# Kernel tuning notes

Hardware: AMD Instinct MI355X
Metric: run time of the kernel (lower is better)

Reference implementation:

```python
import jax, jax.numpy as jnp
import numpy as np

B, S, D, H, E = 4, 1024, 1024, 4096, 8


def setup_inputs() -> dict:
    key = jax.random.key(0)
    ks = jax.random.split(key, 5)
    sd = 1.0 / np.sqrt(D)
    sh = 1.0 / np.sqrt(H)
    x = jax.random.normal(ks[0], (B, S, D), dtype=jnp.float32)
    # stacked expert weights: Linear(D->H), ReLU, Linear(H->D)
    W1 = jax.random.normal(ks[1], (E, D, H), dtype=jnp.float32) * sd
    b1 = jnp.zeros((E, H), dtype=jnp.float32)
    W2 = jax.random.normal(ks[2], (E, H, D), dtype=jnp.float32) * sh
    b2 = jnp.zeros((E, D), dtype=jnp.float32)
    # gate Linear(D->E)
    Wg = jax.random.normal(ks[3], (D, E), dtype=jnp.float32) * sd
    bg = jnp.zeros((E,), dtype=jnp.float32)
    return {"x": x, "W1": W1, "b1": b1, "W2": W2, "b2": b2,
            "Wg": Wg, "bg": bg, "top_k": 2}


def reference(x, W1, b1, W2, b2, Wg, bg, top_k):
    # gating
    gating_scores = jnp.einsum('bsd,de->bse', x, Wg) + bg          # [B,S,E]
    gating_probs = jax.nn.softmax(gating_scores, axis=-1)
    _, top_k_indices = jax.lax.top_k(gating_probs, top_k)          # [B,S,K]
    n_exp = Wg.shape[1]
    # per-token 0/1 mask of selected experts (matches torch sum over k of mask)
    # NOTE: original code multiplies by the binary mask only; top_k_probs are
    # computed but NOT used as combine weights. We reproduce that faithfully.
    sel = jnp.sum(top_k_indices[..., None] == jnp.arange(n_exp), axis=2)  # [B,S,E]
    sel = sel.astype(x.dtype)
    # dense all-experts FFN (as the original does)
    h = jax.nn.relu(jnp.einsum('bsd,edh->bseh', x, W1) + b1)       # [B,S,E,H]
    eo = jnp.einsum('bseh,ehd->bsed', h, W2) + b2                  # [B,S,E,D]
    output = jnp.einsum('bsed,bse->bsd', eo, sel)                  # [B,S,D]
    return (output, gating_scores)
```

## Files before the change

### kernel.cpp

```cpp
#include <hip/hip_runtime.h>
#include <hip/hip_bf16.h>
#include <stdint.h>

#define B_ 4
#define S_ 1024
#define D_ 1024
#define H_ 4096
#define E_ 8
#define T_ (B_*S_)

#define GBM 128
#define BK 64
#define MAXT1 2432
#define MAXT2 1280

typedef __bf16 bf16x8 __attribute__((ext_vector_type(8)));
typedef float f32x4 __attribute__((ext_vector_type(4)));
typedef unsigned short ushort8 __attribute__((ext_vector_type(8)));
typedef unsigned short ushort4v __attribute__((ext_vector_type(4)));

__device__ __forceinline__ unsigned short f2bf(float f) {
  union { float f; uint32_t u; } v; v.f = f;
  uint32_t u = v.u;
  u += 0x7fff + ((u >> 16) & 1);
  return (unsigned short)(u >> 16);
}

__device__ __forceinline__ void gl16(const void* g, void* l) {
  __builtin_amdgcn_global_load_lds(
      (const __attribute__((address_space(1))) void*)g,
      (__attribute__((address_space(3))) void*)l,
      16, 0, 0);
}

__global__ __launch_bounds__(256) void transpose_conv(
    const float* __restrict__ in, unsigned short* __restrict__ outp,
    int R, int C) {
  __shared__ unsigned short tile[64][66];
  const int e = blockIdx.z;
  const size_t eoff = (size_t)e * R * C;
  const int r0 = blockIdx.y * 64, c0 = blockIdx.x * 64;
  const int t = threadIdx.x;
  {
    const int r = t >> 2, cseg = (t & 3) * 16;
    const float4* s4 = (const float4*)(in + eoff + (size_t)(r0 + r) * C + (c0 + cseg));
    float4 v0 = s4[0], v1 = s4[1], v2 = s4[2], v3 = s4[3];
    ushort8 w0, w1;
    w0[0]=f2bf(v0.x); w0[1]=f2bf(v0.y); w0[2]=f2bf(v0.z); w0[3]=f2bf(v0.w);
    w0[4]=f2bf(v1.x); w0[5]=f2bf(v1.y); w0[6]=f2bf(v1.z); w0[7]=f2bf(v1.w);
    w1[0]=f2bf(v2.x); w1[1]=f2bf(v2.y); w1[2]=f2bf(v2.z); w1[3]=f2bf(v2.w);
    w1[4]=f2bf(v3.x); w1[5]=f2bf(v3.y); w1[6]=f2bf(v3.z); w1[7]=f2bf(v3.w);
    *(ushort8*)&tile[r][cseg]     = w0;
    *(ushort8*)&tile[r][cseg + 8] = w1;
  }
  __syncthreads();
  {
    const int c = t >> 2, rseg = (t & 3) * 16;
    ushort8 w0, w1;
#pragma unroll
    for (int j = 0; j < 8; ++j) {
      w0[j] = tile[rseg + j][c];
      w1[j] = tile[rseg + 8 + j][c];
    }
    unsigned short* dst = outp + eoff + (size_t)(c0 + c) * R + (r0 + rseg);
    *(ushort8*)dst       = w0;
    *(ushort8*)(dst + 8) = w1;
  }
}

__global__ __launch_bounds__(256) void gating_kernel(
    const float* __restrict__ x, const float* __restrict__ Wg,
    const float* __restrict__ bg, float* __restrict__ scores,
    unsigned short* __restrict__ xb,
    int* __restrict__ cnt, int* __restrict__ lists) {
  int t = blockIdx.x * 4 + (threadIdx.x >> 6);
  int l = threadIdx.x & 63;
  float acc[E_];
#pragma unroll
  for (int e = 0; e < E_; ++e) acc[e] = 0.f;
  const float* xr = x + (size_t)t * D_;
  unsigned short* xbr = xb + (size_t)t * D_;
  for (int k4 = l * 4; k4 < D_; k4 += 256) {
    float4 xv = *(const float4*)(xr + k4);
    ushort4v wq;
    wq[0] = f2bf(xv.x); wq[1] = f2bf(xv.y); wq[2] = f2bf(xv.z); wq[3] = f2bf(xv.w);
    *(ushort4v*)(xbr + k4) = wq;
#pragma unroll
    for (int q = 0; q < 4; ++q) {
      float xs = (q == 0) ? xv.x : (q == 1) ? xv.y : (q == 2) ? xv.z : xv.w;
      const float4* w = (const float4*)(Wg + (size_t)(k4 + q) * E_);
      float4 w0 = w[0], w1 = w[1];
      acc[0] += xs * w0.x; acc[1] += xs * w0.y; acc[2] += xs * w0.z; acc[3] += xs * w0.w;
      acc[4] += xs * w1.x; acc[5] += xs * w1.y; acc[6] += xs * w1.z; acc[7] += xs * w1.w;
    }
  }
#pragma unroll
  for (int off = 32; off > 0; off >>= 1)
#pragma unroll
    for (int e = 0; e < E_; ++e) acc[e] += __shfl_xor(acc[e], off, 64);
  if (l == 0) {
    float s[E_];
#pragma unroll
    for (int e = 0; e < E_; ++e) {
      s[e] = acc[e] + bg[e];
      scores[(size_t)t * E_ + e] = s[e];
    }
    int i1 = 0; float m1 = -1e30f;
#pragma unroll
    for (int e = 0; e < E_; ++e) if (s[e] > m1) { m1 = s[e]; i1 = e; }
    int i2 = -1; float m2 = -1e30f;
#pragma unroll
    for (int e = 0; e < E_; ++e) if (e != i1 && s[e] > m2) { m2 = s[e]; i2 = e; }
    int p1 = atomicAdd(&cnt[i1], 1); lists[i1 * T_ + p1] = t;
    int p2 = atomicAdd(&cnt[i2], 1); lists[i2 * T_ + p2] = t;
  }
}

__global__ void scan_kernel(const int* __restrict__ cnt, int* __restrict__ off,
                            int* __restrict__ hdr, int* __restrict__ t1tab,
                            int* __restrict__ t2tab) {
  if (threadIdx.x == 0) {
    int o = 0;
    int mtiles[E_];
    for (int e = 0; e < E_; ++e) {
      off[e] = o; o += cnt[e];
      mtiles[e] = (cnt[e] + GBM - 1) / GBM;
    }
    int n1 = 0;
    for (int e = 0; e < E_; ++e)
      for (int nt = 0; nt < H_ / GBM; ++nt)
        for (int mt = 0; mt < mtiles[e]; ++mt)
          t1tab[n1++] = (e << 16) | (mt << 8) | nt;
    int n2 = 0;
    for (int e = 0; e < E_; ++e)
      for (int sp = 0; sp < 2; ++sp)
        for (int nt = 0; nt < D_ / GBM; ++nt)
          for (int mt = 0; mt < mtiles[e]; ++mt)
            t2tab[n2++] = (e << 16) | (mt << 8) | (sp << 6) | nt;
    hdr[0] = n1; hdr[1] = n2;
  }
}

template <int LAYER, int SPLITK>
__global__ __launch_bounds__(256, 4) void ffn_gemm(
    const unsigned short* __restrict__ xb,
    const unsigned short* __restrict__ hbuf,
    const unsigned short* __restrict__ WT,
    const float* __restrict__ bias,
    const int* __restrict__ cnt, const int* __restrict__ off,
    const int* __restrict__ lists,
    const int* __restrict__ tab, const int* __restrict__ hdr,
    unsigned short* __restrict__ hout,
    float* __restrict__ out)
{
  constexpr int K = (LAYER == 1) ? D_ : H_;
  constexpr int N = (LAYER == 1) ? H_ : D_;
  constexpr int KS = K / SPLITK;
  constexpr int NT = KS / BK;

  const int ntask = hdr[LAYER - 1];
  const int b = blockIdx.x;
  if (b >= ntask) return;
  const int q = ntask >> 3, r = ntask & 7;
  const int x = b & 7, ii = b >> 3;
  const int task = (x < r ? x * (q + 1) : r * (q + 1) + (x - r) * q) + ii;

  const int ent = tab[task];
  const int e  = ent >> 16;
  const int m0 = ((ent >> 8) & 0xff) * GBM;
  const int sp = (ent >> 6) & 3;
  const int n0 = (ent & 63) * GBM;
  const int k0 = sp * KS;
  const int count = cnt[e];
  const int oe = off[e];
  const int* lst = lists + e * T_;

  __shared__ unsigned short sA[GBM * BK];
  __shared__ unsigned short sB[GBM * BK];

  const int tid  = threadIdx.x;
  const int lane = tid & 63;
  const int wv   = tid >> 6;
  const int wm   = (wv >> 1) * 64;
  const int wn   = (wv & 1) * 64;

  const int srow   = lane >> 3;
  const int schunk = (lane & 7) * 16;
  const int sgoff  = schunk ^ (srow << 4);

  const char* arow[4];
  const char* brow[4];
#pragma unroll
  for (int i = 0; i < 4; ++i) {
    int rr = i * 32 + wv * 8 + srow;
    int gr = m0 + rr;
    if (LAYER == 1) {
      int tok = (gr < count) ? lst[gr] : lst[m0];
      arow[i] = (const char*)(xb + (size_t)tok * K + k0);
    } else {
      int r2 = (gr < count) ? gr : m0;
      arow[i] = (const char*)(hbuf + (size_t)(oe + r2) * K + k0);
    }
    brow[i] = (const char*)(WT + (size_t)e * N * K + (size_t)(n0 + rr) * K + k0);
  }

  const int lrow = lane & 15;
  const int kg   = lane >> 4;
  const int fswz = (lrow & 7) << 4;

  f32x4 acc[4][4];
#pragma unroll
  for (int i = 0; i < 4; ++i)
#pragma unroll
    for (int j = 0; j < 4; ++j) acc[i][j] = (f32x4){0.f, 0.f, 0.f, 0.f};

#pragma unroll 1
  for (int t = 0; t < NT; ++t) {
    const int kb = t * 128;
#pragma unroll
    for (int i = 0; i < 4; ++i)
      gl16(arow[i] + kb + sgoff, (char*)sA + (i * 32 + wv * 8) * 128);
#pragma unroll
    for (int i = 0; i < 4; ++i)
      gl16(brow[i] + kb + sgoff, (char*)sB + (i * 32 + wv * 8) * 128);
    __syncthreads();
#pragma unroll
    for (int ks = 0; ks < 2; ++ks) {
      bf16x8 af[4], bfm[4];
      const int kbyte = ks * 64 + kg * 16;
#pragma unroll
      for (int i = 0; i < 4; ++i) {
        af[i]  = *(const bf16x8*)((const char*)sA + (wm + i * 16 + lrow) * 128 + (kbyte ^ fswz));
        bfm[i] = *(const bf16x8*)((const char*)sB + (wn + i * 16 + lrow) * 128 + (kbyte ^ fswz));
      }
#pragma unroll
      for (int i = 0; i < 4; ++i)
#pragma unroll
        for (int j = 0; j < 4; ++j)
          acc[i][j] = __builtin_amdgcn_mfma_f32_16x16x32_bf16(af[i], bfm[j], acc[i][j], 0, 0, 0);
    }
    __syncthreads();
  }

  const int rbase = 4 * kg;
#pragma unroll
  for (int i = 0; i < 4; ++i) {
#pragma unroll
    for (int r2 = 0; r2 < 4; ++r2) {
      int row  = wm + i * 16 + rbase + r2;
      int grow = m0 + row;
      if (grow < count) {
#pragma unroll
        for (int j = 0; j < 4; ++j) {
          int col  = wn + j * 16 + lrow;
          int gcol = n0 + col;
          float bv = (SPLITK == 1 || sp == 0) ? bias[(size_t)e * N + gcol] : 0.f;
          float v = acc[i][j][r2] + bv;
          if (LAYER == 1) {
            v = v > 0.f ? v : 0.f;
            hout[(size_t)(oe + grow) * H_ + gcol] = f2bf(v);
          } else {
            int tok = lst[grow];
            atomicAdd(&out[(size_t)tok * D_ + gcol], v);
          }
        }
      }
    }
  }
}

extern "C" void kernel_launch(void* const* d_in, const int* in_sizes, int n_in,
                              void* d_out, int out_size, void* d_ws, size_t ws_size,
                              hipStream_t stream) {
  (void)in_sizes; (void)n_in; (void)out_size; (void)ws_size;
  const float* x  = (const float*)d_in[0];
  const float* W1 = (const float*)d_in[1];
  const float* b1 = (const float*)d_in[2];
  const float* W2 = (const float*)d_in[3];
  const float* b2 = (const float*)d_in[4];
  const float* Wg = (const float*)d_in[5];
  const float* bg = (const float*)d_in[6];

  float* out    = (float*)d_out;
  float* scores = out + (size_t)T_ * D_;

  char* ws = (char*)d_ws;
  int* cnt   = (int*)ws;
  int* off   = (int*)(ws + 32);
  int* hdr   = (int*)(ws + 64);
  int* t1tab = (int*)(ws + 128);
  int* t2tab = (int*)(ws + 10240);
  int* lists = (int*)(ws + 16384);
  unsigned short* xb   = (unsigned short*)(ws + 16384 + 131072);
  unsigned short* hbuf = (unsigned short*)(ws + 16384 + 131072 + 8388608);
  unsigned short* WT   = (unsigned short*)(ws + 16384 + 131072 + 8388608 + 67108864);

  hipMemsetAsync(out, 0, (size_t)T_ * D_ * sizeof(float), stream);
  hipMemsetAsync(cnt, 0, 64, stream);

  gating_kernel<<<T_ / 4, 256, 0, stream>>>(x, Wg, bg, scores, xb, cnt, lists);
  scan_kernel<<<1, 64, 0, stream>>>(cnt, off, hdr, t1tab, t2tab);

  transpose_conv<<<dim3(H_ / 64, D_ / 64, E_), 256, 0, stream>>>(W1, WT, D_, H_);
  ffn_gemm<1, 1><<<MAXT1, 256, 0, stream>>>(
      xb, hbuf, WT, b1, cnt, off, lists, t1tab, hdr, hbuf, nullptr);

  transpose_conv<<<dim3(D_ / 64, H_ / 64, E_), 256, 0, stream>>>(W2, WT, H_, D_);
  ffn_gemm<2, 2><<<MAXT2, 256, 0, stream>>>(
      xb, hbuf, WT, b2, cnt, off, lists, t2tab, hdr, nullptr, out);
}
```

Baseline: 492.8 us.

## Widen GEMM tile to 128x256 and load A fragments directly into registers

The grouped FFN GEMM tile grows from 128x128 to 128x256. The A operand is no longer staged in LDS; each wave loads its A fragments straight from global memory into registers, while B is staged through LDS with twice as many rows. The scan kernel now builds each expert's task-table segment in parallel across threads, and launch bounds drop to 2 blocks per SM to make room for the doubled accumulators. The aim is fewer tasks and more reuse of each LDS B tile per K step, at the cost of uncoalesced direct A loads, lower occupancy and coarser load balance.

```diff
diff --git a/kernel.cpp b/kernel.cpp
--- a/kernel.cpp
+++ b/kernel.cpp
@@ -10,9 +10,10 @@
 #define T_ (B_*S_)
 
 #define GBM 128
+#define GBN 256
 #define BK 64
-#define MAXT1 2432
-#define MAXT2 1280
+#define MAXT1 1216
+#define MAXT2 640
 
 typedef __bf16 bf16x8 __attribute__((ext_vector_type(8)));
 typedef float f32x4 __attribute__((ext_vector_type(4)));
@@ -119,30 +120,38 @@
 __global__ void scan_kernel(const int* __restrict__ cnt, int* __restrict__ off,
                             int* __restrict__ hdr, int* __restrict__ t1tab,
                             int* __restrict__ t2tab) {
-  if (threadIdx.x == 0) {
-    int o = 0;
-    int mtiles[E_];
+  const int l = threadIdx.x;
+  int offl[E_], mt[E_];
+  int o = 0;
+  for (int e = 0; e < E_; ++e) {
+    offl[e] = o; o += cnt[e];
+    mt[e] = (cnt[e] + GBM - 1) / GBM;
+  }
+  if (l < E_) {
+    int s1 = 0, s2 = 0;
+    for (int e = 0; e < l; ++e) { s1 += mt[e] * (H_ / GBN); s2 += mt[e] * 2 * (D_ / GBN); }
+    int n1 = s1;
+    for (int nt = 0; nt < H_ / GBN; ++nt)
+      for (int m = 0; m < mt[l]; ++m)
+        t1tab[n1++] = (l << 16) | (m << 8) | nt;
+    int n2 = s2;
+    for (int sp = 0; sp < 2; ++sp)
+      for (int nt = 0; nt < D_ / GBN; ++nt)
+        for (int m = 0; m < mt[l]; ++m)
+          t2tab[n2++] = (l << 16) | (m << 8) | (sp << 6) | nt;
+  }
+  if (l == 0) {
+    int s1 = 0, s2 = 0;
     for (int e = 0; e < E_; ++e) {
-      off[e] = o; o += cnt[e];
-      mtiles[e] = (cnt[e] + GBM - 1) / GBM;
-    }
-    int n1 = 0;
-    for (int e = 0; e < E_; ++e)
-      for (int nt = 0; nt < H_ / GBM; ++nt)
-        for (int mt = 0; mt < mtiles[e]; ++mt)
-          t1tab[n1++] = (e << 16) | (mt << 8) | nt;
-    int n2 = 0;
-    for (int e = 0; e < E_; ++e)
-      for (int sp = 0; sp < 2; ++sp)
-        for (int nt = 0; nt < D_ / GBM; ++nt)
-          for (int mt = 0; mt < mtiles[e]; ++mt)
-            t2tab[n2++] = (e << 16) | (mt << 8) | (sp << 6) | nt;
-    hdr[0] = n1; hdr[1] = n2;
+      s1 += mt[e] * (H_ / GBN); s2 += mt[e] * 2 * (D_ / GBN);
+      off[e] = offl[e];
+    }
+    hdr[0] = s1; hdr[1] = s2;
   }
 }
 
 template <int LAYER, int SPLITK>
-__global__ __launch_bounds__(256, 4) void ffn_gemm(
+__global__ __launch_bounds__(256, 2) void ffn_gemm(
     const unsigned short* __restrict__ xb,
     const unsigned short* __restrict__ hbuf,
     const unsigned short* __restrict__ WT,
@@ -169,75 +178,78 @@
   const int e  = ent >> 16;
   const int m0 = ((ent >> 8) & 0xff) * GBM;
   const int sp = (ent >> 6) & 3;
-  const int n0 = (ent & 63) * GBM;
+  const int n0 = (ent & 63) * GBN;
   const int k0 = sp * KS;
   const int count = cnt[e];
   const int oe = off[e];
   const int* lst = lists + e * T_;
 
-  __shared__ unsigned short sA[GBM * BK];
-  __shared__ unsigned short sB[GBM * BK];
+  __shared__ unsigned short sB[GBN * BK];
 
   const int tid  = threadIdx.x;
   const int lane = tid & 63;
   const int wv   = tid >> 6;
   const int wm   = (wv >> 1) * 64;
-  const int wn   = (wv & 1) * 64;
+  const int wn   = (wv & 1) * 128;
+
+  const int lrow = lane & 15;
+  const int kg   = lane >> 4;
+  const int fswz = (lrow & 7) << 4;
+
+  const unsigned short* aptr[4];
+#pragma unroll
+  for (int i = 0; i < 4; ++i) {
+    int gr = m0 + wm + i * 16 + lrow;
+    if (LAYER == 1) {
+      int tok = (gr < count) ? lst[gr] : lst[m0];
+      aptr[i] = xb + (size_t)tok * K + k0 + kg * 8;
+    } else {
+      int r2 = (gr < count) ? gr : m0;
+      aptr[i] = hbuf + (size_t)(oe + r2) * K + k0 + kg * 8;
+    }
+  }
 
   const int srow   = lane >> 3;
   const int schunk = (lane & 7) * 16;
   const int sgoff  = schunk ^ (srow << 4);
-
-  const char* arow[4];
-  const char* brow[4];
-#pragma unroll
-  for (int i = 0; i < 4; ++i) {
+  const char* brow[8];
+#pragma unroll
+  for (int i = 0; i < 8; ++i) {
     int rr = i * 32 + wv * 8 + srow;
-    int gr = m0 + rr;
-    if (LAYER == 1) {
-      int tok = (gr < count) ? lst[gr] : lst[m0];
-      arow[i] = (const char*)(xb + (size_t)tok * K + k0);
-    } else {
-      int r2 = (gr < count) ? gr : m0;
-      arow[i] = (const char*)(hbuf + (size_t)(oe + r2) * K + k0);
-    }
     brow[i] = (const char*)(WT + (size_t)e * N * K + (size_t)(n0 + rr) * K + k0);
   }
 
-  const int lrow = lane & 15;
-  const int kg   = lane >> 4;
-  const int fswz = (lrow & 7) << 4;
-
-  f32x4 acc[4][4];
+  f32x4 acc[4][8];
 #pragma unroll
   for (int i = 0; i < 4; ++i)
 #pragma unroll
-    for (int j = 0; j < 4; ++j) acc[i][j] = (f32x4){0.f, 0.f, 0.f, 0.f};
+    for (int j = 0; j < 8; ++j) acc[i][j] = (f32x4){0.f, 0.f, 0.f, 0.f};
 
 #pragma unroll 1
   for (int t = 0; t < NT; ++t) {
-    const int kb = t * 128;
-#pragma unroll
-    for (int i = 0; i < 4; ++i)
-      gl16(arow[i] + kb + sgoff, (char*)sA + (i * 32 + wv * 8) * 128);
-#pragma unroll
-    for (int i = 0; i < 4; ++i)
-      gl16(brow[i] + kb + sgoff, (char*)sB + (i * 32 + wv * 8) * 128);
+    const int kel = t * BK;
+    bf16x8 af[4][2];
+#pragma unroll
+    for (int i = 0; i < 4; ++i) {
+      af[i][0] = *(const bf16x8*)(aptr[i] + kel);
+      af[i][1] = *(const bf16x8*)(aptr[i] + kel + 32);
+    }
+#pragma unroll
+    for (int i = 0; i < 8; ++i)
+      gl16(brow[i] + kel * 2 + sgoff, (char*)sB + (i * 32 + wv * 8) * 128);
     __syncthreads();
 #pragma unroll
     for (int ks = 0; ks < 2; ++ks) {
-      bf16x8 af[4], bfm[4];
+      bf16x8 bfm[8];
       const int kbyte = ks * 64 + kg * 16;
 #pragma unroll
-      for (int i = 0; i < 4; ++i) {
-        af[i]  = *(const bf16x8*)((const char*)sA + (wm + i * 16 + lrow) * 128 + (kbyte ^ fswz));
-        bfm[i] = *(const bf16x8*)((const char*)sB + (wn + i * 16 + lrow) * 128 + (kbyte ^ fswz));
-      }
+      for (int j = 0; j < 8; ++j)
+        bfm[j] = *(const bf16x8*)((const char*)sB + (wn + j * 16 + lrow) * 128 + (kbyte ^ fswz));
 #pragma unroll
       for (int i = 0; i < 4; ++i)
 #pragma unroll
-        for (int j = 0; j < 4; ++j)
-          acc[i][j] = __builtin_amdgcn_mfma_f32_16x16x32_bf16(af[i], bfm[j], acc[i][j], 0, 0, 0);
+        for (int j = 0; j < 8; ++j)
+          acc[i][j] = __builtin_amdgcn_mfma_f32_16x16x32_bf16(af[i][ks], bfm[j], acc[i][j], 0, 0, 0);
     }
     __syncthreads();
   }
@@ -251,7 +263,7 @@
       int grow = m0 + row;
       if (grow < count) {
 #pragma unroll
-        for (int j = 0; j < 4; ++j) {
+        for (int j = 0; j < 8; ++j) {
           int col  = wn + j * 16 + lrow;
           int gcol = n0 + col;
           float bv = (SPLITK == 1 || sp == 0) ? bias[(size_t)e * N + gcol] : 0.f;
@@ -289,7 +301,7 @@
   int* off   = (int*)(ws + 32);
   int* hdr   = (int*)(ws + 64);
   int* t1tab = (int*)(ws + 128);
-  int* t2tab = (int*)(ws + 10240);
+  int* t2tab = (int*)(ws + 128 + 4 * MAXT1);
   int* lists = (int*)(ws + 16384);
   unsigned short* xb   = (unsigned short*)(ws + 16384 + 131072);
   unsigned short* hbuf = (unsigned short*)(ws + 16384 + 131072 + 8388608);
```

Result: slower. 571.5 us (+16.0%).

## Fuse weight transposes into gating and GEMM launches, parallelize scan

Applied to the files above, without the earlier changes.

Folds the W1 transpose/convert into the gating kernel as extra blocks, and the W2 transpose into the layer-1 GEMM launch as trailing blocks writing to a separate buffer when workspace allows. The task-table scan is spread across 256 threads instead of one. The aim is fewer launches and overlap of bandwidth-bound transposes with compute. It needs more workspace and falls back to the old path if that is unavailable, and the GEMM blocks now declare shared memory before an early-exit branch.

```diff
diff --git a/kernel.cpp b/kernel.cpp
--- a/kernel.cpp
+++ b/kernel.cpp
@@ -13,6 +13,8 @@
 #define BK 64
 #define MAXT1 2432
 #define MAXT2 1280
+#define T1BLK 8192
+#define T2BLK 8192
 
 typedef __bf16 bf16x8 __attribute__((ext_vector_type(8)));
 typedef float f32x4 __attribute__((ext_vector_type(4)));
@@ -33,14 +35,11 @@
       16, 0, 0);
 }
 
-__global__ __launch_bounds__(256) void transpose_conv(
+__device__ __forceinline__ void transpose_tile(
     const float* __restrict__ in, unsigned short* __restrict__ outp,
-    int R, int C) {
-  __shared__ unsigned short tile[64][66];
-  const int e = blockIdx.z;
+    int R, int C, int e, int r0, int c0, int t,
+    unsigned short (*tile)[66]) {
   const size_t eoff = (size_t)e * R * C;
-  const int r0 = blockIdx.y * 64, c0 = blockIdx.x * 64;
-  const int t = threadIdx.x;
   {
     const int r = t >> 2, cseg = (t & 3) * 16;
     const float4* s4 = (const float4*)(in + eoff + (size_t)(r0 + r) * C + (c0 + cseg));
@@ -68,11 +67,28 @@
   }
 }
 
-__global__ __launch_bounds__(256) void gating_kernel(
+__global__ __launch_bounds__(256) void transpose_conv(
+    const float* __restrict__ in, unsigned short* __restrict__ outp,
+    int R, int C) {
+  __shared__ unsigned short tile[64][66];
+  transpose_tile(in, outp, R, C, blockIdx.z, blockIdx.y * 64, blockIdx.x * 64,
+                 threadIdx.x, tile);
+}
+
+__global__ __launch_bounds__(256) void gate_t1_kernel(
     const float* __restrict__ x, const float* __restrict__ Wg,
     const float* __restrict__ bg, float* __restrict__ scores,
     unsigned short* __restrict__ xb,
-    int* __restrict__ cnt, int* __restrict__ lists) {
+    int* __restrict__ cnt, int* __restrict__ lists,
+    const float* __restrict__ W1, unsigned short* __restrict__ WT1) {
+  __shared__ unsigned short tile[64][66];
+  if (blockIdx.x >= T_ / 4) {
+    int bid = blockIdx.x - T_ / 4;
+    int e = bid >> 10, rem = bid & 1023;
+    int cx = rem & 63, ry = rem >> 6;
+    transpose_tile(W1, WT1, D_, H_, e, ry * 64, cx * 64, threadIdx.x, tile);
+    return;
+  }
   int t = blockIdx.x * 4 + (threadIdx.x >> 6);
   int l = threadIdx.x & 63;
   float acc[E_];
@@ -119,29 +135,39 @@
 __global__ void scan_kernel(const int* __restrict__ cnt, int* __restrict__ off,
                             int* __restrict__ hdr, int* __restrict__ t1tab,
                             int* __restrict__ t2tab) {
-  if (threadIdx.x == 0) {
-    int o = 0;
-    int mtiles[E_];
+  int mt[E_], offl[E_];
+  int o = 0;
+  for (int e = 0; e < E_; ++e) {
+    offl[e] = o; o += cnt[e];
+    mt[e] = (cnt[e] + GBM - 1) / GBM;
+  }
+  const int t = threadIdx.x;
+  {
+    int e = t >> 5, nt = t & 31;
+    int s1 = 0;
+    for (int q = 0; q < e; ++q) s1 += mt[q] * (H_ / GBM);
+    int base = s1 + nt * mt[e];
+    for (int m = 0; m < mt[e]; ++m) t1tab[base + m] = (e << 16) | (m << 8) | nt;
+  }
+  if (t < 128) {
+    int e = t >> 4, idx = t & 15, sp = idx >> 3, nt = idx & 7;
+    int s2 = 0;
+    for (int q = 0; q < e; ++q) s2 += mt[q] * 2 * (D_ / GBM);
+    int base = s2 + (sp * (D_ / GBM) + nt) * mt[e];
+    for (int m = 0; m < mt[e]; ++m)
+      t2tab[base + m] = (e << 16) | (m << 8) | (sp << 6) | nt;
+  }
+  if (t == 0) {
+    int s1 = 0, s2 = 0;
     for (int e = 0; e < E_; ++e) {
-      off[e] = o; o += cnt[e];
-      mtiles[e] = (cnt[e] + GBM - 1) / GBM;
-    }
-    int n1 = 0;
-    for (int e = 0; e < E_; ++e)
-      for (int nt = 0; nt < H_ / GBM; ++nt)
-        for (int mt = 0; mt < mtiles[e]; ++mt)
-          t1tab[n1++] = (e << 16) | (mt << 8) | nt;
-    int n2 = 0;
-    for (int e = 0; e < E_; ++e)
-      for (int sp = 0; sp < 2; ++sp)
-        for (int nt = 0; nt < D_ / GBM; ++nt)
-          for (int mt = 0; mt < mtiles[e]; ++mt)
-            t2tab[n2++] = (e << 16) | (mt << 8) | (sp << 6) | nt;
-    hdr[0] = n1; hdr[1] = n2;
-  }
-}
-
-template <int LAYER, int SPLITK>
+      s1 += mt[e] * (H_ / GBM); s2 += mt[e] * 2 * (D_ / GBM);
+      off[e] = offl[e];
+    }
+    hdr[0] = s1; hdr[1] = s2;
+  }
+}
+
+template <int LAYER, int SPLITK, bool FUSET2>
 __global__ __launch_bounds__(256, 4) void ffn_gemm(
     const unsigned short* __restrict__ xb,
     const unsigned short* __restrict__ hbuf,
@@ -151,12 +177,25 @@
     const int* __restrict__ lists,
     const int* __restrict__ tab, const int* __restrict__ hdr,
     unsigned short* __restrict__ hout,
-    float* __restrict__ out)
+    float* __restrict__ out,
+    const float* __restrict__ Wsrc, unsigned short* __restrict__ WTdst)
 {
   constexpr int K = (LAYER == 1) ? D_ : H_;
   constexpr int N = (LAYER == 1) ? H_ : D_;
   constexpr int KS = K / SPLITK;
   constexpr int NT = KS / BK;
+
+  __shared__ unsigned short sA[GBM * BK];
+  __shared__ unsigned short sB[GBM * BK];
+
+  if (FUSET2 && blockIdx.x >= MAXT1) {
+    int bid = blockIdx.x - MAXT1;
+    int e = bid >> 10, rem = bid & 1023;
+    int cx = rem & 15, ry = rem >> 4;
+    transpose_tile(Wsrc, WTdst, H_, D_, e, ry * 64, cx * 64, threadIdx.x,
+                   (unsigned short (*)[66])sA);
+    return;
+  }
 
   const int ntask = hdr[LAYER - 1];
   const int b = blockIdx.x;
@@ -174,9 +213,6 @@
   const int count = cnt[e];
   const int oe = off[e];
   const int* lst = lists + e * T_;
-
-  __shared__ unsigned short sA[GBM * BK];
-  __shared__ unsigned short sB[GBM * BK];
 
   const int tid  = threadIdx.x;
   const int lane = tid & 63;
@@ -272,7 +308,7 @@
 extern "C" void kernel_launch(void* const* d_in, const int* in_sizes, int n_in,
                               void* d_out, int out_size, void* d_ws, size_t ws_size,
                               hipStream_t stream) {
-  (void)in_sizes; (void)n_in; (void)out_size; (void)ws_size;
+  (void)in_sizes; (void)n_in; (void)out_size;
   const float* x  = (const float*)d_in[0];
   const float* W1 = (const float*)d_in[1];
   const float* b1 = (const float*)d_in[2];
@@ -291,21 +327,30 @@
   int* t1tab = (int*)(ws + 128);
   int* t2tab = (int*)(ws + 10240);
   int* lists = (int*)(ws + 16384);
-  unsigned short* xb   = (unsigned short*)(ws + 16384 + 131072);
-  unsigned short* hbuf = (unsigned short*)(ws + 16384 + 131072 + 8388608);
-  unsigned short* WT   = (unsigned short*)(ws + 16384 + 131072 + 8388608 + 67108864);
+  const size_t BASE = 16384 + 131072;
+  unsigned short* xb   = (unsigned short*)(ws + BASE);
+  unsigned short* hbuf = (unsigned short*)(ws + BASE + 8388608);
+  unsigned short* WT1  = (unsigned short*)(ws + BASE + 8388608 + 67108864);
+  const size_t NEED2 = BASE + 8388608 + 67108864ull * 3;
+  const bool fuse = (ws_size >= NEED2);
+  unsigned short* WT2 = fuse ? (WT1 + 67108864 / 2) : WT1;
 
   hipMemsetAsync(out, 0, (size_t)T_ * D_ * sizeof(float), stream);
   hipMemsetAsync(cnt, 0, 64, stream);
 
-  gating_kernel<<<T_ / 4, 256, 0, stream>>>(x, Wg, bg, scores, xb, cnt, lists);
-  scan_kernel<<<1, 64, 0, stream>>>(cnt, off, hdr, t1tab, t2tab);
-
-  transpose_conv<<<dim3(H_ / 64, D_ / 64, E_), 256, 0, stream>>>(W1, WT, D_, H_);
-  ffn_gemm<1, 1><<<MAXT1, 256, 0, stream>>>(
-      xb, hbuf, WT, b1, cnt, off, lists, t1tab, hdr, hbuf, nullptr);
-
-  transpose_conv<<<dim3(D_ / 64, H_ / 64, E_), 256, 0, stream>>>(W2, WT, H_, D_);
-  ffn_gemm<2, 2><<<MAXT2, 256, 0, stream>>>(
-      xb, hbuf, WT, b2, cnt, off, lists, t2tab, hdr, nullptr, out);
-}
+  gate_t1_kernel<<<T_ / 4 + T1BLK, 256, 0, stream>>>(
+      x, Wg, bg, scores, xb, cnt, lists, W1, WT1);
+  scan_kernel<<<1, 256, 0, stream>>>(cnt, off, hdr, t1tab, t2tab);
+
+  if (fuse) {
+    ffn_gemm<1, 1, true><<<MAXT1 + T2BLK, 256, 0, stream>>>(
+        xb, hbuf, WT1, b1, cnt, off, lists, t1tab, hdr, hbuf, nullptr, W2, WT2);
+  } else {
+    ffn_gemm<1, 1, false><<<MAXT1, 256, 0, stream>>>(
+        xb, hbuf, WT1, b1, cnt, off, lists, t1tab, hdr, hbuf, nullptr, nullptr, nullptr);
+    transpose_conv<<<dim3(D_ / 64, H_ / 64, E_), 256, 0, stream>>>(W2, WT2, H_, D_);
+  }
+
+  ffn_gemm<2, 2, false><<<MAXT2, 256, 0, stream>>>(
+      xb, hbuf, WT2, b2, cnt, off, lists, t2tab, hdr, nullptr, out, nullptr, nullptr);
+}
```

Result: faster. 411.3 us (median of 3 runs) (-16.5%).
